# Kernel optimization log

Hardware: AMD Instinct MI355X
Metric: run time of the kernel (lower is better)

## Reference

```python
import jax, jax.numpy as jnp
import numpy as np

N_HEADS = 16
N_KV_HEADS = 4
N_EMBED = 2048
HEAD_DIM = 128
SECTIONS = [16, 24, 24, 16, 24, 24]


def _process_rotary(c):
    # c: [3, B, T, HEAD_DIM] -> [B, 1, T, HEAD_DIM]
    splits = np.cumsum(SECTIONS)[:-1]
    secs = jnp.split(c, splits, axis=-1)
    out = jnp.concatenate([s[i % 3] for i, s in enumerate(secs)], axis=-1)
    return out[:, None]  # add head axis


def _rotate_half(x):
    x1, x2 = jnp.split(x, 2, axis=-1)
    return jnp.concatenate([-x2, x1], axis=-1)


def setup_inputs() -> dict:
    key = jax.random.key(0)
    ks = jax.random.split(key, 12)
    B, T = 1, 2048
    s = 0.02
    return {
        "x": jax.random.normal(ks[0], (B, T, N_EMBED), jnp.float32),
        "cos": jax.random.uniform(ks[1], (3, B, T, HEAD_DIM), jnp.float32),
        "sin": jax.random.uniform(ks[2], (3, B, T, HEAD_DIM), jnp.float32),
        "Wq": jax.random.normal(ks[3], (N_EMBED, N_EMBED), jnp.float32) * s,
        "bq": jax.random.normal(ks[4], (N_EMBED,), jnp.float32) * s,
        "Wk": jax.random.normal(ks[5], (N_EMBED, N_KV_HEADS * HEAD_DIM), jnp.float32) * s,
        "bk": jax.random.normal(ks[6], (N_KV_HEADS * HEAD_DIM,), jnp.float32) * s,
        "Wv": jax.random.normal(ks[7], (N_EMBED, N_KV_HEADS * HEAD_DIM), jnp.float32) * s,
        "bv": jax.random.normal(ks[8], (N_KV_HEADS * HEAD_DIM,), jnp.float32) * s,
        "Wo": jax.random.normal(ks[9], (N_EMBED, N_EMBED), jnp.float32) * s,
    }


def reference(x, cos, sin, Wq, bq, Wk, bk, Wv, bv, Wo):
    B, T, C = x.shape
    H, Hkv, D = N_HEADS, N_KV_HEADS, HEAD_DIM
    q = (x @ Wq + bq).reshape(B, T, H, D).transpose(0, 2, 1, 3)    # [B,H,T,D]
    k = (x @ Wk + bk).reshape(B, T, Hkv, D).transpose(0, 2, 1, 3)  # [B,Hkv,T,D]
    v = (x @ Wv + bv).reshape(B, T, Hkv, D).transpose(0, 2, 1, 3)
    # multi-section rope (cos/sin are 4-dim -> custom path)
    c = _process_rotary(cos)
    s = _process_rotary(sin)
    q = q * c + _rotate_half(q) * s
    k = k * c + _rotate_half(k) * s
    present_k, present_v = k, v
    # GQA expansion (repeat_interleave over head axis)
    r = H // Hkv
    k = jnp.repeat(k, r, axis=1)
    v = jnp.repeat(v, r, axis=1)
    # causal SDPA
    scores = jnp.einsum("bhqd,bhkd->bhqk", q, k) / jnp.sqrt(jnp.float32(D))
    causal = jnp.tril(jnp.ones((T, T), dtype=bool))
    scores = jnp.where(causal, scores, jnp.finfo(scores.dtype).min)
    attn = jax.nn.softmax(scores, axis=-1)
    y = jnp.einsum("bhqk,bhkd->bhqd", attn, v)
    y = y.transpose(0, 2, 1, 3).reshape(B, T, C)
    y = y @ Wo
    return (y, present_k, present_v)
```

## Files before the change

### kernel.cpp

```cpp
#include <hip/hip_runtime.h>

typedef unsigned short u16;
typedef unsigned int u32;
typedef __attribute__((ext_vector_type(4))) float f32x4;
typedef __attribute__((ext_vector_type(8))) __bf16 bf16x8;
typedef __attribute__((ext_vector_type(4))) u16 u16x4;
typedef __attribute__((ext_vector_type(2))) u32 u32x2;


__device__ __forceinline__ u16 f2bf(float f) {
  union { float f; unsigned u; } v; v.f = f;
  unsigned r = v.u + 0x7fffu + ((v.u >> 16) & 1u);
  return (u16)(r >> 16);
}

__device__ __forceinline__ u32 pack_bf2(float a, float b) {
  union { float f; unsigned u; } x, y;
  x.f = a; y.f = b;
#if __has_builtin(__builtin_amdgcn_perm)
  return __builtin_amdgcn_perm(y.u + 0x8000u, x.u + 0x8000u, 0x07060302u);
#else
  return (u32)((x.u + 0x8000u) >> 16) | ((y.u + 0x8000u) & 0xffff0000u);
#endif
}

__device__ __forceinline__ void stage16(const void* g, void* l) {
#if __has_builtin(__builtin_amdgcn_global_load_lds)
  __builtin_amdgcn_global_load_lds((const __attribute__((address_space(1))) void*)g,
                                   (__attribute__((address_space(3))) void*)l, 16, 0, 0);
#else
  *(f32x4*)l = *(const f32x4*)g;
#endif
}

__device__ __forceinline__ f32x4 mfma16(bf16x8 a, bf16x8 b, f32x4 c) {
  return __builtin_amdgcn_mfma_f32_16x16x32_bf16(a, b, c, 0, 0, 0);
}

__device__ __forceinline__ float fexp2(float x) {
#if __has_builtin(__builtin_amdgcn_exp2f)
  return __builtin_amdgcn_exp2f(x);
#else
  return exp2f(x);
#endif
}

__device__ __forceinline__ int rope_ch(int d) {
  int dd = (d < 64) ? d : d - 64;
  return (dd < 16) ? 0 : (dd < 40 ? 1 : 2);
}


__global__ void yuna_convert_prep(const float* __restrict__ in, u16* __restrict__ out,
                                  const float* __restrict__ cosp, const float* __restrict__ sinp,
                                  float* __restrict__ csel, float* __restrict__ ssel) {
  int b = blockIdx.x;
  if (b < 4096) {
    int i = b * 256 + threadIdx.x;
    f32x4 v = ((const f32x4*)in)[i];
    u16x4 o;
    o.x = f2bf(v.x); o.y = f2bf(v.y); o.z = f2bf(v.z); o.w = f2bf(v.w);
    ((u16x4*)out)[i] = o;
  } else {
    int i = (b - 4096) * 256 + threadIdx.x;
    int i4 = i * 4;
    int t = i4 >> 7, d = i4 & 127;
    f32x4 c, s;
#pragma unroll
    for (int j = 0; j < 4; ++j) {
      int ch = rope_ch(d + j);
      c[j] = cosp[(size_t)ch * 262144 + (size_t)t * 128 + d + j];
      s[j] = sinp[(size_t)ch * 262144 + (size_t)t * 128 + d + j];
    }
    ((f32x4*)csel)[i] = c;
    ((f32x4*)ssel)[i] = s;
  }
}

__global__ void yuna_prep_weights(const float* __restrict__ Wq, const float* __restrict__ Wk,
                                  const float* __restrict__ Wv, const float* __restrict__ Wo,
                                  u16* __restrict__ Wb, u16* __restrict__ Wob) {
  __shared__ float tile[64][65];
  const int mat = blockIdx.z;
  const float* W;
  u16* out;
  int N;
  if (mat == 0)      { W = Wq; out = Wb;                          N = 2048; }
  else if (mat == 1) { W = Wk; out = Wb + (size_t)2048 * 2048;    N = 512; }
  else if (mat == 2) { W = Wv; out = Wb + (size_t)2560 * 2048;    N = 512; }
  else               { W = Wo; out = Wob;                         N = 2048; }
  int k0 = blockIdx.x * 64, n0 = blockIdx.y * 64;
  if (n0 >= N) return;
  int tx = threadIdx.x & 63, ty = threadIdx.x >> 6;
#pragma unroll
  for (int j = 0; j < 64; j += 4)
    tile[ty + j][tx] = W[(size_t)(k0 + ty + j) * N + n0 + tx];
  __syncthreads();
#pragma unroll
  for (int j = 0; j < 64; j += 4)
    out[(size_t)(n0 + ty + j) * 2048 + k0 + tx] = f2bf(tile[tx][ty + j]);
}

__global__ __launch_bounds__(256, 3) void yuna_gemm_qkv(
    const u16* __restrict__ A, const u16* __restrict__ Bt,
    const float* __restrict__ bq, const float* __restrict__ bk, const float* __restrict__ bv,
    const float* __restrict__ csel, const float* __restrict__ ssel,
    u16* __restrict__ qb, u16* __restrict__ kb, u16* __restrict__ vtb,
    float* __restrict__ pk, float* __restrict__ pv) {
  const int K = 2048;
  __shared__ __align__(16) char smem[49152];
  const int tid = threadIdx.x;
  const int wave = tid >> 6, lane = tid & 63;
  const int lrow = lane & 15, lkg = lane >> 4;
  const int m0 = blockIdx.x * 64;
  const int by = blockIdx.y;
  const int n0 = by * 128;
  const int sw = lrow & 7;

  const int srow = tid >> 3;
  const int ssc = (tid & 7) ^ ((tid >> 3) & 7);
  const size_t abase = (size_t)(m0 + srow) * K + ssc * 8;
  const size_t bbase = (size_t)(n0 + srow) * K + ssc * 8;

  const f32x4 fzero = {0.f, 0.f, 0.f, 0.f};
  f32x4 acc[4][2];
#pragma unroll
  for (int mi = 0; mi < 4; ++mi) { acc[mi][0] = fzero; acc[mi][1] = fzero; }

#pragma unroll
  for (int it = 0; it < 2; ++it)
    stage16(A + abase + (size_t)it * 32 * K, smem + (tid + it * 256) * 16);
#pragma unroll
  for (int it = 0; it < 4; ++it)
    stage16(Bt + bbase + (size_t)it * 32 * K, smem + 16384 + (tid + it * 256) * 16);

  for (int k0 = 0, ki = 0; k0 < K; k0 += 64, ++ki) {
    const int cur = ki & 1;
    const char* Asb = smem + cur * 8192;
    const char* Bsb = smem + 16384 + cur * 16384;
    if (k0 + 64 < K) {
      char* Asn = smem + (cur ^ 1) * 8192;
      char* Bsn = smem + 16384 + (cur ^ 1) * 16384;
#pragma unroll
      for (int it = 0; it < 2; ++it)
        stage16(A + abase + (size_t)it * 32 * K + k0 + 64, Asn + (tid + it * 256) * 16);
#pragma unroll
      for (int it = 0; it < 4; ++it)
        stage16(Bt + bbase + (size_t)it * 32 * K + k0 + 64, Bsn + (tid + it * 256) * 16);
      asm volatile("s_waitcnt vmcnt(6)\n\ts_barrier" ::: "memory");
    } else {
      asm volatile("s_waitcnt vmcnt(0)\n\ts_barrier" ::: "memory");
    }
#pragma unroll
    for (int kk = 0; kk < 2; ++kk) {
      const int cof = ((kk * 4 + lkg) ^ sw) << 4;
      bf16x8 af[4], bfr[2];
#pragma unroll
      for (int mi = 0; mi < 4; ++mi)
        af[mi] = *(const bf16x8*)(Asb + (mi * 16 + lrow) * 128 + cof);
#pragma unroll
      for (int ni = 0; ni < 2; ++ni)
        bfr[ni] = *(const bf16x8*)(Bsb + (wave * 16 + ni * 64 + lrow) * 128 + cof);
#pragma unroll
      for (int mi = 0; mi < 4; ++mi)
#pragma unroll
        for (int ni = 0; ni < 2; ++ni)
          acc[mi][ni] = mfma16(af[mi], bfr[ni], acc[mi][ni]);
    }
    asm volatile("s_barrier" ::: "memory");
  }

  if (by >= 20) {
    const int kvh = by - 20;
#pragma unroll
    for (int mi = 0; mi < 4; ++mi)
#pragma unroll
      for (int ni = 0; ni < 2; ++ni) {
        int d = wave * 16 + ni * 64 + lrow;
        float bb = bv[kvh * 128 + d];
        int mb = mi * 16 + lkg * 4;
        float v0 = acc[mi][ni][0] + bb, v1 = acc[mi][ni][1] + bb;
        float v2 = acc[mi][ni][2] + bb, v3 = acc[mi][ni][3] + bb;
        size_t pb = ((size_t)(kvh * 2048 + m0 + mb)) * 128 + d;
        pv[pb] = v0; pv[pb + 128] = v1; pv[pb + 256] = v2; pv[pb + 384] = v3;
        u16x4 w;
        w.x = f2bf(v0); w.y = f2bf(v1); w.z = f2bf(v2); w.w = f2bf(v3);
        *(u16x4*)(vtb + ((size_t)(kvh * 128 + d)) * 2048 + m0 + mb) = w;
      }
  } else {
    const float QSCALE = 1.4426950408889634f * 0.08838834764831845f;
    const bool isQ = (by < 16);
    const int h = isQ ? by : (by - 16);
    const float* bias = isQ ? bq : bk;
    const int dlo = wave * 16 + lrow;
    const float blo = bias[h * 128 + dlo];
    const float bhi = bias[h * 128 + dlo + 64];
#pragma unroll
    for (int mi = 0; mi < 4; ++mi) {
      const int tb = m0 + mi * 16 + lkg * 4;
#pragma unroll
      for (int r = 0; r < 4; ++r) {
        const int t = tb + r;
        float a = acc[mi][0][r] + blo;
        float b = acc[mi][1][r] + bhi;
        size_t cb = (size_t)t * 128 + dlo;
        float cl = csel[cb], sl = ssel[cb];
        float ch = csel[cb + 64], sh = ssel[cb + 64];
        float lo = a * cl - b * sl;
        float hi = b * ch + a * sh;
        size_t o = (((size_t)(h * 2048 + t)) << 7) + dlo;
        if (isQ) {
          qb[o] = f2bf(lo * QSCALE);
          qb[o + 64] = f2bf(hi * QSCALE);
        } else {
          kb[o] = f2bf(lo);
          kb[o + 64] = f2bf(hi);
          pk[o] = lo; pk[o + 64] = hi;
        }
      }
    }
  }
}

__global__ __launch_bounds__(256, 3) void yuna_gemm_out(
    const u16* __restrict__ A, const u16* __restrict__ Bt, float* __restrict__ C) {
  const int K = 2048;
  __shared__ __align__(16) char smem[49152];
  const int tid = threadIdx.x;
  const int wave = tid >> 6, lane = tid & 63;
  const int lrow = lane & 15, lkg = lane >> 4;
  const int m0 = blockIdx.x * 64;
  const int n0 = blockIdx.y * 128;
  const int wc = wave * 32;
  const int sw = lrow & 7;

  const int srow = tid >> 3;
  const int ssc = (tid & 7) ^ ((tid >> 3) & 7);
  const size_t abase = (size_t)(m0 + srow) * K + ssc * 8;
  const size_t bbase = (size_t)(n0 + srow) * K + ssc * 8;

  const f32x4 fzero = {0.f, 0.f, 0.f, 0.f};
  f32x4 acc[4][2];
#pragma unroll
  for (int mi = 0; mi < 4; ++mi) { acc[mi][0] = fzero; acc[mi][1] = fzero; }

#pragma unroll
  for (int it = 0; it < 2; ++it)
    stage16(A + abase + (size_t)it * 32 * K, smem + (tid + it * 256) * 16);
#pragma unroll
  for (int it = 0; it < 4; ++it)
    stage16(Bt + bbase + (size_t)it * 32 * K, smem + 16384 + (tid + it * 256) * 16);

  for (int k0 = 0, ki = 0; k0 < K; k0 += 64, ++ki) {
    const int cur = ki & 1;
    const char* Asb = smem + cur * 8192;
    const char* Bsb = smem + 16384 + cur * 16384;
    if (k0 + 64 < K) {
      char* Asn = smem + (cur ^ 1) * 8192;
      char* Bsn = smem + 16384 + (cur ^ 1) * 16384;
#pragma unroll
      for (int it = 0; it < 2; ++it)
        stage16(A + abase + (size_t)it * 32 * K + k0 + 64, Asn + (tid + it * 256) * 16);
#pragma unroll
      for (int it = 0; it < 4; ++it)
        stage16(Bt + bbase + (size_t)it * 32 * K + k0 + 64, Bsn + (tid + it * 256) * 16);
      asm volatile("s_waitcnt vmcnt(6)\n\ts_barrier" ::: "memory");
    } else {
      asm volatile("s_waitcnt vmcnt(0)\n\ts_barrier" ::: "memory");
    }
#pragma unroll
    for (int kk = 0; kk < 2; ++kk) {
      const int cof = ((kk * 4 + lkg) ^ sw) << 4;
      bf16x8 af[4], bfr[2];
#pragma unroll
      for (int mi = 0; mi < 4; ++mi)
        af[mi] = *(const bf16x8*)(Asb + (mi * 16 + lrow) * 128 + cof);
#pragma unroll
      for (int ni = 0; ni < 2; ++ni)
        bfr[ni] = *(const bf16x8*)(Bsb + (wc + ni * 16 + lrow) * 128 + cof);
#pragma unroll
      for (int mi = 0; mi < 4; ++mi)
#pragma unroll
        for (int ni = 0; ni < 2; ++ni)
          acc[mi][ni] = mfma16(af[mi], bfr[ni], acc[mi][ni]);
    }
    asm volatile("s_barrier" ::: "memory");
  }
#pragma unroll
  for (int mi = 0; mi < 4; ++mi)
#pragma unroll
    for (int ni = 0; ni < 2; ++ni) {
      int d = wc + ni * 16 + lrow;
      int mb = mi * 16 + lkg * 4;
#pragma unroll
      for (int r = 0; r < 4; ++r)
        C[(size_t)(m0 + mb + r) * 2048 + n0 + d] = acc[mi][ni][r];
    }
}

__global__ __launch_bounds__(256, 2) void yuna_flash_attn(
    const u16* __restrict__ Q,
    const u16* __restrict__ Kb,
    const u16* __restrict__ Vt,
    u16* __restrict__ Y) {
  __shared__ __align__(16) u16 Ks[2][64 * 128];
  __shared__ __align__(16) u16 Vs[2][128 * 64];
  __shared__ __align__(16) u16 Ps[64 * 64];
  const int h = blockIdx.x;
  const int yb = blockIdx.y;
  const int qb = (yb < 16) ? yb : 47 - yb;
  const int kvh = h >> 2;
  const int tid = threadIdx.x, wave = tid >> 6, lane = tid & 63;
  const int lrow = lane & 15, lkg = lane >> 4;
  const int m = wave * 16 + lrow;
  const int sw = lrow & 7;

  const int krow = tid >> 4;
  const int ksc = (tid & 15) ^ ((tid >> 4) & 7);
  const size_t kbase0 = ((size_t)(kvh * 2048 + krow) << 7) + ksc * 8;
  const int vrow = tid >> 3;
  const int vsc = (tid & 7) ^ ((tid >> 3) & 7);
  const size_t vbase0 = (size_t)(kvh * 128 + vrow) * 2048 + vsc * 8;

  bf16x8 qf[4];
#pragma unroll
  for (int kk = 0; kk < 4; ++kk)
    qf[kk] = *(const bf16x8*)(Q + (((size_t)h * 2048 + qb * 64 + m) << 7) + kk * 32 + lkg * 8);

  const f32x4 fzero = {0.f, 0.f, 0.f, 0.f};
  f32x4 o[8];
#pragma unroll
  for (int dt = 0; dt < 8; ++dt) o[dt] = fzero;
  float m_i = -1e30f, l_i = 0.f;

  const int nkb = qb + 1;

#pragma unroll
  for (int it = 0; it < 4; ++it)
    stage16(Kb + kbase0 + ((size_t)(it * 16) << 7), (char*)Ks[0] + (tid + it * 256) * 16);
#pragma unroll
  for (int it = 0; it < 4; ++it)
    stage16(Vt + vbase0 + (size_t)it * 32 * 2048, (char*)Vs[0] + (tid + it * 256) * 16);

  for (int kb = 0; kb < nkb; ++kb) {
    const int cur = kb & 1;
    const char* Ksb = (const char*)Ks[cur];
    const char* Vsb = (const char*)Vs[cur];
    if (kb + 1 < nkb) {
      char* Ksn = (char*)Ks[cur ^ 1];
      char* Vsn = (char*)Vs[cur ^ 1];
#pragma unroll
      for (int it = 0; it < 4; ++it)
        stage16(Kb + kbase0 + ((size_t)((kb + 1) * 64 + it * 16) << 7), Ksn + (tid + it * 256) * 16);
#pragma unroll
      for (int it = 0; it < 4; ++it)
        stage16(Vt + vbase0 + (size_t)it * 32 * 2048 + (kb + 1) * 64, Vsn + (tid + it * 256) * 16);
      asm volatile("s_waitcnt vmcnt(8)\n\ts_barrier" ::: "memory");
    } else {
      asm volatile("s_waitcnt vmcnt(0)\n\ts_barrier" ::: "memory");
    }

    f32x4 s[4];
#pragma unroll
    for (int nt = 0; nt < 4; ++nt) s[nt] = fzero;
#pragma unroll
    for (int kk = 0; kk < 4; ++kk) {
      const int cof = ((kk * 4 + lkg) ^ sw) << 4;
      bf16x8 kf[4];
#pragma unroll
      for (int nt = 0; nt < 4; ++nt)
        kf[nt] = *(const bf16x8*)(Ksb + (nt * 16 + lrow) * 256 + cof);
#pragma unroll
      for (int nt = 0; nt < 4; ++nt)
        s[nt] = mfma16(kf[nt], qf[kk], s[nt]);
    }
    if (kb == qb) {
#pragma unroll
      for (int nt = 0; nt < 4; ++nt)
#pragma unroll
        for (int r = 0; r < 4; ++r)
          if (nt * 16 + lkg * 4 + r > m) s[nt][r] = -1e30f;
    }

    float mx = -1e30f;
#pragma unroll
    for (int nt = 0; nt < 4; ++nt)
#pragma unroll
      for (int r = 0; r < 4; ++r) mx = fmaxf(mx, s[nt][r]);
    mx = fmaxf(mx, __shfl_xor(mx, 16));
    mx = fmaxf(mx, __shfl_xor(mx, 32));
    float mnew = fmaxf(m_i, mx);
    float alpha = fexp2(m_i - mnew);
    m_i = mnew;
    float ps = 0.f;
    const int hh = lkg & 1;
#pragma unroll
    for (int nt = 0; nt < 4; ++nt) {
      float p0 = fexp2(s[nt][0] - mnew);
      float p1 = fexp2(s[nt][1] - mnew);
      float p2 = fexp2(s[nt][2] - mnew);
      float p3 = fexp2(s[nt][3] - mnew);
      ps += (p0 + p1) + (p2 + p3);
      u32x2 pk2;
      pk2.x = pack_bf2(p0, p1);
      pk2.y = pack_bf2(p2, p3);
      int cc = 2 * nt + (lkg >> 1);
      *(u32x2*)((char*)Ps + m * 128 + ((cc ^ (m & 7)) << 4) + hh * 8) = pk2;
    }
    ps += __shfl_xor(ps, 16);
    ps += __shfl_xor(ps, 32);
    l_i = l_i * alpha + ps;
#pragma unroll
    for (int dt = 0; dt < 8; ++dt) o[dt] *= alpha;

#pragma unroll
    for (int kk = 0; kk < 2; ++kk) {
      const int cof = ((kk * 4 + lkg) ^ sw) << 4;
      bf16x8 pf = *(const bf16x8*)((char*)Ps + m * 128 + cof);
      bf16x8 vf[8];
#pragma unroll
      for (int dt = 0; dt < 8; ++dt)
        vf[dt] = *(const bf16x8*)(Vsb + (dt * 16 + lrow) * 128 + cof);
#pragma unroll
      for (int dt = 0; dt < 8; ++dt)
        o[dt] = mfma16(vf[dt], pf, o[dt]);
    }
    asm volatile("s_barrier" ::: "memory");
  }

  __syncthreads();
  {
    float inv = 1.f / l_i;
    const int hh = lkg & 1;
#pragma unroll
    for (int dt = 0; dt < 8; ++dt) {
      u32x2 w2;
      w2.x = pack_bf2(o[dt][0] * inv, o[dt][1] * inv);
      w2.y = pack_bf2(o[dt][2] * inv, o[dt][3] * inv);
      int cc = 2 * dt + (lkg >> 1);
      *(u32x2*)((char*)Ks[0] + m * 256 + ((cc ^ (m & 7)) << 4) + hh * 8) = w2;
    }
  }
  __syncthreads();
#pragma unroll
  for (int it = 0; it < 4; ++it) {
    int c = tid + it * 256;
    int row = c >> 4, cc = c & 15;
    f32x4 v = *(const f32x4*)((const char*)Ks[0] + row * 256 + ((cc ^ (row & 7)) << 4));
    *(f32x4*)(Y + (size_t)(qb * 64 + row) * 2048 + h * 128 + cc * 8) = v;
  }
}


extern "C" void kernel_launch(void* const* d_in, const int* in_sizes, int n_in,
                              void* d_out, int out_size, void* d_ws, size_t ws_size,
                              hipStream_t stream) {
  const float* x = (const float*)d_in[0];
  const float* cosp = (const float*)d_in[1];
  const float* sinp = (const float*)d_in[2];
  const float* Wq = (const float*)d_in[3];
  const float* bq = (const float*)d_in[4];
  const float* Wk = (const float*)d_in[5];
  const float* bk = (const float*)d_in[6];
  const float* Wv = (const float*)d_in[7];
  const float* bv = (const float*)d_in[8];
  const float* Wo = (const float*)d_in[9];
  float* out = (float*)d_out;
  float* out_k = out + 4194304;
  float* out_v = out + 5242880;

  char* ws = (char*)d_ws;
  u16* xb   = (u16*)(ws + 0);
  u16* Wb   = (u16*)(ws + 8388608);
  u16* Wob  = (u16*)(ws + 20971520);
  float* csel = (float*)(ws + 29360128);
  float* ssel = (float*)(ws + 30408704);
  u16* qbuf = (u16*)(ws + 54525952);
  u16* kbuf = (u16*)(ws + 62914560);
  u16* vtb  = (u16*)(ws + 65011712);
  u16* yat  = (u16*)(ws + 67108864);

  yuna_convert_prep<<<4352, 256, 0, stream>>>(x, xb, cosp, sinp, csel, ssel);
  yuna_prep_weights<<<dim3(32, 32, 4), 256, 0, stream>>>(Wq, Wk, Wv, Wo, Wb, Wob);
  yuna_gemm_qkv<<<dim3(32, 24), 256, 0, stream>>>(xb, Wb, bq, bk, bv, csel, ssel,
                                                  qbuf, kbuf, vtb, out_k, out_v);
  yuna_flash_attn<<<dim3(16, 32), 256, 0, stream>>>(qbuf, kbuf, vtb, yat);
  yuna_gemm_out<<<dim3(32, 16), 256, 0, stream>>>(yat, Wob, out);
}
```

Measured before the change: 233.3 us.

## Merge prep kernels, interleave causal q-block order, add lazy rescale and setprio

```diff
diff --git a/kernel.cpp b/kernel.cpp
--- a/kernel.cpp
+++ b/kernel.cpp
@@ -51,18 +51,42 @@
 }
 
 
-__global__ void yuna_convert_prep(const float* __restrict__ in, u16* __restrict__ out,
-                                  const float* __restrict__ cosp, const float* __restrict__ sinp,
-                                  float* __restrict__ csel, float* __restrict__ ssel) {
-  int b = blockIdx.x;
-  if (b < 4096) {
-    int i = b * 256 + threadIdx.x;
-    f32x4 v = ((const f32x4*)in)[i];
+__global__ void yuna_prep(const float* __restrict__ x, u16* __restrict__ xb,
+                          const float* __restrict__ cosp, const float* __restrict__ sinp,
+                          float* __restrict__ csel, float* __restrict__ ssel,
+                          const float* __restrict__ Wq, const float* __restrict__ Wk,
+                          const float* __restrict__ Wv, const float* __restrict__ Wo,
+                          u16* __restrict__ Wb, u16* __restrict__ Wob) {
+  __shared__ float tile[64][65];
+  const int bid = blockIdx.x;
+  if (bid < 4096) {
+    const int mat = bid >> 10;
+    const int rem = bid & 1023;
+    const float* W;
+    u16* out;
+    int N;
+    if (mat == 0)      { W = Wq; out = Wb;                          N = 2048; }
+    else if (mat == 1) { W = Wk; out = Wb + (size_t)2048 * 2048;    N = 512; }
+    else if (mat == 2) { W = Wv; out = Wb + (size_t)2560 * 2048;    N = 512; }
+    else               { W = Wo; out = Wob;                         N = 2048; }
+    int k0 = (rem & 31) << 6, n0 = (rem >> 5) << 6;
+    if (n0 >= N) return;
+    int tx = threadIdx.x & 63, ty = threadIdx.x >> 6;
+#pragma unroll
+    for (int j = 0; j < 64; j += 4)
+      tile[ty + j][tx] = W[(size_t)(k0 + ty + j) * N + n0 + tx];
+    __syncthreads();
+#pragma unroll
+    for (int j = 0; j < 64; j += 4)
+      out[(size_t)(n0 + ty + j) * 2048 + k0 + tx] = f2bf(tile[tx][ty + j]);
+  } else if (bid < 8192) {
+    int i = (bid - 4096) * 256 + threadIdx.x;
+    f32x4 v = ((const f32x4*)x)[i];
     u16x4 o;
     o.x = f2bf(v.x); o.y = f2bf(v.y); o.z = f2bf(v.z); o.w = f2bf(v.w);
-    ((u16x4*)out)[i] = o;
+    ((u16x4*)xb)[i] = o;
   } else {
-    int i = (b - 4096) * 256 + threadIdx.x;
+    int i = (bid - 8192) * 256 + threadIdx.x;
     int i4 = i * 4;
     int t = i4 >> 7, d = i4 & 127;
     f32x4 c, s;
@@ -75,30 +99,6 @@
     ((f32x4*)csel)[i] = c;
     ((f32x4*)ssel)[i] = s;
   }
-}
-
-__global__ void yuna_prep_weights(const float* __restrict__ Wq, const float* __restrict__ Wk,
-                                  const float* __restrict__ Wv, const float* __restrict__ Wo,
-                                  u16* __restrict__ Wb, u16* __restrict__ Wob) {
-  __shared__ float tile[64][65];
-  const int mat = blockIdx.z;
-  const float* W;
-  u16* out;
-  int N;
-  if (mat == 0)      { W = Wq; out = Wb;                          N = 2048; }
-  else if (mat == 1) { W = Wk; out = Wb + (size_t)2048 * 2048;    N = 512; }
-  else if (mat == 2) { W = Wv; out = Wb + (size_t)2560 * 2048;    N = 512; }
-  else               { W = Wo; out = Wob;                         N = 2048; }
-  int k0 = blockIdx.x * 64, n0 = blockIdx.y * 64;
-  if (n0 >= N) return;
-  int tx = threadIdx.x & 63, ty = threadIdx.x >> 6;
-#pragma unroll
-  for (int j = 0; j < 64; j += 4)
-    tile[ty + j][tx] = W[(size_t)(k0 + ty + j) * N + n0 + tx];
-  __syncthreads();
-#pragma unroll
-  for (int j = 0; j < 64; j += 4)
-    out[(size_t)(n0 + ty + j) * 2048 + k0 + tx] = f2bf(tile[tx][ty + j]);
 }
 
 __global__ __launch_bounds__(256, 3) void yuna_gemm_qkv(
@@ -308,7 +308,7 @@
   __shared__ __align__(16) u16 Ps[64 * 64];
   const int h = blockIdx.x;
   const int yb = blockIdx.y;
-  const int qb = (yb < 16) ? yb : 47 - yb;
+  const int qb = (yb & 1) ? (yb >> 1) : 31 - (yb >> 1);
   const int kvh = h >> 2;
   const int tid = threadIdx.x, wave = tid >> 6, lane = tid & 63;
   const int lrow = lane & 15, lkg = lane >> 4;
@@ -363,6 +363,7 @@
     f32x4 s[4];
 #pragma unroll
     for (int nt = 0; nt < 4; ++nt) s[nt] = fzero;
+    __builtin_amdgcn_s_setprio(1);
 #pragma unroll
     for (int kk = 0; kk < 4; ++kk) {
       const int cof = ((kk * 4 + lkg) ^ sw) << 4;
@@ -374,6 +375,7 @@
       for (int nt = 0; nt < 4; ++nt)
         s[nt] = mfma16(kf[nt], qf[kk], s[nt]);
     }
+    __builtin_amdgcn_s_setprio(0);
     if (kb == qb) {
 #pragma unroll
       for (int nt = 0; nt < 4; ++nt)
@@ -389,17 +391,22 @@
       for (int r = 0; r < 4; ++r) mx = fmaxf(mx, s[nt][r]);
     mx = fmaxf(mx, __shfl_xor(mx, 16));
     mx = fmaxf(mx, __shfl_xor(mx, 32));
-    float mnew = fmaxf(m_i, mx);
-    float alpha = fexp2(m_i - mnew);
-    m_i = mnew;
+    if (__any(mx > m_i + 8.0f)) {
+      float mnew = fmaxf(m_i, mx);
+      float alpha = fexp2(m_i - mnew);
+      m_i = mnew;
+      l_i *= alpha;
+#pragma unroll
+      for (int dt = 0; dt < 8; ++dt) o[dt] *= alpha;
+    }
     float ps = 0.f;
     const int hh = lkg & 1;
 #pragma unroll
     for (int nt = 0; nt < 4; ++nt) {
-      float p0 = fexp2(s[nt][0] - mnew);
-      float p1 = fexp2(s[nt][1] - mnew);
-      float p2 = fexp2(s[nt][2] - mnew);
-      float p3 = fexp2(s[nt][3] - mnew);
+      float p0 = fexp2(s[nt][0] - m_i);
+      float p1 = fexp2(s[nt][1] - m_i);
+      float p2 = fexp2(s[nt][2] - m_i);
+      float p3 = fexp2(s[nt][3] - m_i);
       ps += (p0 + p1) + (p2 + p3);
       u32x2 pk2;
       pk2.x = pack_bf2(p0, p1);
@@ -409,10 +416,9 @@
     }
     ps += __shfl_xor(ps, 16);
     ps += __shfl_xor(ps, 32);
-    l_i = l_i * alpha + ps;
-#pragma unroll
-    for (int dt = 0; dt < 8; ++dt) o[dt] *= alpha;
-
+    l_i += ps;
+
+    __builtin_amdgcn_s_setprio(1);
 #pragma unroll
     for (int kk = 0; kk < 2; ++kk) {
       const int cof = ((kk * 4 + lkg) ^ sw) << 4;
@@ -425,6 +431,7 @@
       for (int dt = 0; dt < 8; ++dt)
         o[dt] = mfma16(vf[dt], pf, o[dt]);
     }
+    __builtin_amdgcn_s_setprio(0);
     asm volatile("s_barrier" ::: "memory");
   }
 
@@ -480,8 +487,8 @@
   u16* vtb  = (u16*)(ws + 65011712);
   u16* yat  = (u16*)(ws + 67108864);
 
-  yuna_convert_prep<<<4352, 256, 0, stream>>>(x, xb, cosp, sinp, csel, ssel);
-  yuna_prep_weights<<<dim3(32, 32, 4), 256, 0, stream>>>(Wq, Wk, Wv, Wo, Wb, Wob);
+  yuna_prep<<<8448, 256, 0, stream>>>(x, xb, cosp, sinp, csel, ssel,
+                                      Wq, Wk, Wv, Wo, Wb, Wob);
   yuna_gemm_qkv<<<dim3(32, 24), 256, 0, stream>>>(xb, Wb, bq, bk, bv, csel, ssel,
                                                   qbuf, kbuf, vtb, out_k, out_v);
   yuna_flash_attn<<<dim3(16, 32), 256, 0, stream>>>(qbuf, kbuf, vtb, yat);
```

New measurement: 221.4 us. 1.05x faster.
